# Performance work log

Hardware: AMD Instinct MI355X
Metric: run time of the kernel (lower is better)

Reference implementation:

```python
import jax, jax.numpy as jnp
import numpy as np

NUM_NODES = 100000
NUM_NEIGHS = 64
FEAT = 128
BATCH = 16384
NUM_SAMPLES = 16


def setup_inputs() -> dict:
    key = jax.random.key(0)
    k_ids, k_feat, k_adj = jax.random.split(key, 3)
    ids = jax.random.randint(k_ids, (BATCH,), 0, NUM_NODES, dtype=jnp.int64 if jax.config.jax_enable_x64 else jnp.int32)
    features = jax.random.normal(k_feat, (NUM_NODES, FEAT), dtype=jnp.float32)
    adj_info = jax.random.randint(k_adj, (NUM_NODES, NUM_NEIGHS), 0, NUM_NODES, dtype=jnp.int32)
    return {
        "ids": ids,
        "num_samples": NUM_SAMPLES,
        "features": features,
        "batch_size": BATCH,
        "adj_info": adj_info,
    }


def reference(ids, num_samples, features, batch_size, adj_info):
    # Gather adjacency rows and center-node features
    adj_lists = jnp.take(adj_info, ids, axis=0)            # [B, K]
    node_features = jnp.take(features, ids, axis=0)        # [B, F]
    neighbor_feature = jnp.take(features, adj_lists, axis=0)  # [B, K, F]
    # Euclidean distance center -> each neighbor (broadcast instead of tile)
    diff = node_features[:, None, :] - neighbor_feature    # [B, K, F]
    distance = jnp.sqrt(jnp.sum(diff * diff, axis=-1))     # [B, K]
    prob = jnp.exp(-distance)
    prob = prob / jnp.sum(prob, axis=-1, keepdims=True)    # [B, K]
    # Categorical sampling of num_samples neighbors per row
    logits = jnp.log(prob)
    skey = jax.random.key(42)
    samples_idx = jax.random.categorical(skey, logits, axis=-1, shape=(num_samples, batch_size)).T  # [B, S]
    selected = jnp.take_along_axis(adj_lists, samples_idx, axis=1)  # [B, S]
    return selected
```

## Files before the change

kernel.cpp:

```cpp
#include <hip/hip_runtime.h>
#include <stdint.h>

#define NB 16384
#define NK 64
#define NF 128
#define NS 16
#define RPB 4

__device__ __forceinline__ float xla_exp_f32(float x_in) {
#pragma clang fp contract(off)
  const float exp_hi = 88.3762626647950f;
  const float exp_lo = -88.3762626647949f;
  const float log2ef = 1.44269504088896341f;
  const float c1 = 0.693359375f;
  const float c2 = -2.12194440e-4f;
  const float p0 = 1.9875691500E-4f;
  const float p1 = 1.3981999507E-3f;
  const float p2 = 8.3334519073E-3f;
  const float p3 = 4.1665795894E-2f;
  const float p4 = 1.6666665459E-1f;
  const float p5 = 5.0000001201E-1f;

  float x = fminf(fmaxf(x_in, exp_lo), exp_hi);
  float fx = floorf(fmaf(x, log2ef, 0.5f));
  float tmp = c1 * fx;
  float z2 = c2 * fx;
  x = x - tmp;
  x = x - z2;
  float z = x * x;
  float y = fmaf(x, p0, p1);
  y = fmaf(y, x, p2);
  y = fmaf(y, x, p3);
  y = fmaf(y, x, p4);
  y = fmaf(y, x, p5);
  y = fmaf(y, z, x);
  y = y + 1.0f;
  int n = (int)fx;
  float two_n = __int_as_float((n + 127) << 23);
  return fmaxf(y * two_n, x_in);
}

__device__ __forceinline__ float xla_log_f32(float x_in) {
#pragma clang fp contract(off)
  const float sqrthf = 0.707106781186547524f;
  const float p0 = 7.0376836292E-2f;
  const float p1 = -1.1514610310E-1f;
  const float p2 = 1.1676998740E-1f;
  const float p3 = -1.2420140846E-1f;
  const float p4 = 1.4249322787E-1f;
  const float p5 = -1.6668057665E-1f;
  const float p6 = 2.0000714765E-1f;
  const float p7 = -2.4999993993E-1f;
  const float p8 = 3.3333331174E-1f;
  const float q1 = -2.12194440e-4f;
  const float q2 = 0.693359375f;

  float t = fmaxf(x_in, __uint_as_float(0x00800000u));
  uint32_t bits = __float_as_uint(t);
  float e = (float)((int)(bits >> 23) - 0x7f) + 1.0f;
  float m = __uint_as_float((bits & 0x007fffffu) | 0x3f000000u);
  bool lt = (m < sqrthf);
  float madd = lt ? m : 0.0f;
  e = e - (lt ? 1.0f : 0.0f);
  m = (m + madd) - 1.0f;

  float z = m * m;
  float y = fmaf(m, p0, p1);
  y = fmaf(y, m, p2);
  y = fmaf(y, m, p3);
  y = fmaf(y, m, p4);
  y = fmaf(y, m, p5);
  y = fmaf(y, m, p6);
  y = fmaf(y, m, p7);
  y = fmaf(y, m, p8);
  y = y * m;
  y = y * z;
  y = fmaf(e, q1, y);
  y = y - 0.5f * z;
  float r = m + y;
  r = fmaf(e, q2, r);
  return r;
}

__device__ __forceinline__ void threefry2x32_k42(uint32_t c0, uint32_t c1,
                                                 uint32_t& o0, uint32_t& o1) {
  const uint32_t k0 = 0u, k1 = 42u;
  const uint32_t k2 = k0 ^ k1 ^ 0x1BD11BDAu;
  uint32_t x0 = c0 + k0, x1 = c1 + k1;
#define TF_R(r) { x0 += x1; x1 = (x1 << (r)) | (x1 >> (32 - (r))); x1 ^= x0; }
  TF_R(13) TF_R(15) TF_R(26) TF_R(6)
  x0 += k1; x1 += k2 + 1u;
  TF_R(17) TF_R(29) TF_R(16) TF_R(24)
  x0 += k2; x1 += k0 + 2u;
  TF_R(13) TF_R(15) TF_R(26) TF_R(6)
  x0 += k0; x1 += k1 + 3u;
  TF_R(17) TF_R(29) TF_R(16) TF_R(24)
  x0 += k1; x1 += k2 + 4u;
  TF_R(13) TF_R(15) TF_R(26) TF_R(6)
  x0 += k2; x1 += k0 + 5u;
#undef TF_R
  o0 = x0; o1 = x1;
}

__device__ __forceinline__ uint32_t jax_random_bits32(uint32_t m) {
  uint32_t a, b;
  threefry2x32_k42(0u, m, a, b);
  return a ^ b;
}

__device__ __forceinline__ float gumbel_from_bits(uint32_t bits) {
#pragma clang fp contract(off)
  const float tiny = 1.17549435e-38f;
  float f = __uint_as_float((bits >> 9) | 0x3f800000u) - 1.0f;
  float u = fmaxf(tiny, f + tiny);
  return -xla_log_f32(-xla_log_f32(u));
}

__global__ void __launch_bounds__(256)
dns_kernel(const int* __restrict__ ids, const float* __restrict__ features,
           const int* __restrict__ adj, int* __restrict__ out) {
#pragma clang fp contract(off)
  __shared__ __align__(16) char sbuf[RPB][8192];
  __shared__ __align__(16) float fc[RPB][NF];
  __shared__ __align__(16) float esh[RPB][NK];
  __shared__ int nsh[RPB][NK];
  __shared__ float zb[RPB][NS][4];
  __shared__ int ib[RPB][NS][4];

  const int wave = threadIdx.x >> 6;
  const int k = threadIdx.x & 63;
  const int b = blockIdx.x * RPB + wave;
  const int center = ids[b];

  if (k < NF / 4)
    ((float4*)fc[wave])[k] = ((const float4*)(features + (size_t)center * NF))[k];
  nsh[wave][k] = adj[(size_t)center * NK + k];
  asm volatile("s_waitcnt lgkmcnt(0)" ::: "memory");

  const int rg = k >> 3;
  const int eg = k & 7;
  float acc = 0.0f;
#pragma unroll 1
  for (int q = 0; q < 4; ++q) {
#pragma unroll
    for (int i = 0; i < 8; ++i) {
      const int r = i * 8 + rg;
      const int rn = nsh[wave][r];
      const int esrc = eg ^ (r & 7);
      const float4* g = (const float4*)features + ((size_t)rn * (NF / 4) + q * 8 + esrc);
      __builtin_amdgcn_global_load_lds(
          (const __attribute__((address_space(1))) void*)g,
          (__attribute__((address_space(3))) void*)(sbuf[wave] + i * 1024),
          16, 0, 0);
    }
    asm volatile("s_waitcnt vmcnt(0)" ::: "memory");
#pragma unroll
    for (int j2 = 0; j2 < 8; ++j2) {
      const float4 v = *(const float4*)(sbuf[wave] + k * 128 + ((j2 ^ (k & 7)) << 4));
      const int j = q * 8 + j2;
      float d0 = fc[wave][4 * j + 0] - v.x; acc = acc + d0 * d0;
      float d1 = fc[wave][4 * j + 1] - v.y; acc = acc + d1 * d1;
      float d2 = fc[wave][4 * j + 2] - v.z; acc = acc + d2 * d2;
      float d3 = fc[wave][4 * j + 3] - v.w; acc = acc + d3 * d3;
    }
    asm volatile("s_waitcnt lgkmcnt(0)" ::: "memory");
  }

  const float ev = xla_exp_f32(-sqrtf(acc));
  esh[wave][k] = ev;
  asm volatile("s_waitcnt lgkmcnt(0)" ::: "memory");

  float s = 0.0f;
  const float4* e4 = (const float4*)esh[wave];
#pragma unroll
  for (int i = 0; i < NK / 4; ++i) {
    float4 v = e4[i];
    s = s + v.x; s = s + v.y; s = s + v.z; s = s + v.w;
  }
  const float logit = xla_log_f32(ev / s);

  float (*zsh)[NK + 1] = (float (*)[NK + 1])(void*)sbuf[wave];
#pragma unroll
  for (int ss = 0; ss < NS; ++ss) {
    uint32_t m = (uint32_t)((ss * NB + b) * NK + k);
    zsh[ss][k] = gumbel_from_bits(jax_random_bits32(m)) + logit;
  }
  asm volatile("s_waitcnt lgkmcnt(0)" ::: "memory");

  const int samp = k >> 2;
  const int sub = k & 3;
  const int kbase = sub * 16;
  float best = zsh[samp][kbase];
  int bi = kbase;
#pragma unroll 1
  for (int j = 1; j < 16; ++j) {
    const float v = zsh[samp][kbase + j];
    if (v > best) { best = v; bi = kbase + j; }
  }
  zb[wave][samp][sub] = best;
  ib[wave][samp][sub] = bi;
  asm volatile("s_waitcnt lgkmcnt(0)" ::: "memory");

  if (sub == 0) {
    float bb = zb[wave][samp][0];
    int bbi = ib[wave][samp][0];
#pragma unroll
    for (int qq = 1; qq < 4; ++qq) {
      const float v = zb[wave][samp][qq];
      if (v > bb) { bb = v; bbi = ib[wave][samp][qq]; }
    }
    out[b * NS + samp] = nsh[wave][bbi];
  }
}

extern "C" void kernel_launch(void* const* d_in, const int* in_sizes, int n_in,
                              void* d_out, int out_size, void* d_ws, size_t ws_size,
                              hipStream_t stream) {
  const int* ids = (const int*)d_in[0];
  const float* features = (const float*)d_in[2];
  const int* adj = (const int*)d_in[4];
  int* out = (int*)d_out;
  (void)in_sizes; (void)n_in; (void)out_size; (void)d_ws; (void)ws_size;

  dns_kernel<<<dim3(NB / RPB), dim3(64 * RPB), 0, stream>>>(ids, features, adj, out);
}
```

Baseline: 91.85 us.

## Double-buffer neighbor feature gathers into LDS across eight chunks

Measured after the change: 103.8 us. 1.13x slower.

```diff
diff --git a/kernel.cpp b/kernel.cpp
--- a/kernel.cpp
+++ b/kernel.cpp
@@ -116,6 +116,9 @@
   return -xla_log_f32(-xla_log_f32(u));
 }
 
+#define AS1 __attribute__((address_space(1)))
+#define AS3 __attribute__((address_space(3)))
+
 __global__ void __launch_bounds__(256)
 dns_kernel(const int* __restrict__ ids, const float* __restrict__ features,
            const int* __restrict__ adj, int* __restrict__ out) {
@@ -131,40 +134,61 @@
   const int k = threadIdx.x & 63;
   const int b = blockIdx.x * RPB + wave;
   const int center = ids[b];
+  char* sb = sbuf[wave];
 
   if (k < NF / 4)
     ((float4*)fc[wave])[k] = ((const float4*)(features + (size_t)center * NF))[k];
   nsh[wave][k] = adj[(size_t)center * NK + k];
   asm volatile("s_waitcnt lgkmcnt(0)" ::: "memory");
 
-  const int rg = k >> 3;
-  const int eg = k & 7;
+  const int kq = k >> 2;
+  const int esrc = (k & 3) ^ ((k >> 3) & 3);
+  const float4* f4 = (const float4*)features;
+  const float4* g0 = f4 + (size_t)nsh[wave][0 * 16 + kq] * (NF / 4) + esrc;
+  const float4* g1 = f4 + (size_t)nsh[wave][1 * 16 + kq] * (NF / 4) + esrc;
+  const float4* g2 = f4 + (size_t)nsh[wave][2 * 16 + kq] * (NF / 4) + esrc;
+  const float4* g3 = f4 + (size_t)nsh[wave][3 * 16 + kq] * (NF / 4) + esrc;
+
+#define STAGE(half)                                                         \
+  do {                                                                      \
+    __builtin_amdgcn_global_load_lds((const AS1 void*)g0,                   \
+        (AS3 void*)(sb + (half)), 16, 0, 0);                                \
+    __builtin_amdgcn_global_load_lds((const AS1 void*)g1,                   \
+        (AS3 void*)(sb + (half) + 1024), 16, 0, 0);                         \
+    __builtin_amdgcn_global_load_lds((const AS1 void*)g2,                   \
+        (AS3 void*)(sb + (half) + 2048), 16, 0, 0);                         \
+    __builtin_amdgcn_global_load_lds((const AS1 void*)g3,                   \
+        (AS3 void*)(sb + (half) + 3072), 16, 0, 0);                         \
+    g0 += 4; g1 += 4; g2 += 4; g3 += 4;                                     \
+  } while (0)
+
+  const int S4 = ((k >> 1) & 3) << 4;
+  const float4* fc4 = (const float4*)fc[wave];
   float acc = 0.0f;
+#define CONSUME(cc, half)                                                   \
+  do {                                                                      \
+    const char* rb = sb + (half) + k * 64;                                  \
+    _Pragma("unroll")                                                       \
+    for (int t = 0; t < 4; ++t) {                                           \
+      const float4 v = *(const float4*)(rb + ((t << 4) ^ S4));              \
+      const float4 f = fc4[(cc) * 4 + t];                                   \
+      float d0 = f.x - v.x; acc = acc + d0 * d0;                            \
+      float d1 = f.y - v.y; acc = acc + d1 * d1;                            \
+      float d2 = f.z - v.z; acc = acc + d2 * d2;                            \
+      float d3 = f.w - v.w; acc = acc + d3 * d3;                            \
+    }                                                                       \
+  } while (0)
+
+  STAGE(0);
 #pragma unroll 1
-  for (int q = 0; q < 4; ++q) {
-#pragma unroll
-    for (int i = 0; i < 8; ++i) {
-      const int r = i * 8 + rg;
-      const int rn = nsh[wave][r];
-      const int esrc = eg ^ (r & 7);
-      const float4* g = (const float4*)features + ((size_t)rn * (NF / 4) + q * 8 + esrc);
-      __builtin_amdgcn_global_load_lds(
-          (const __attribute__((address_space(1))) void*)g,
-          (__attribute__((address_space(3))) void*)(sbuf[wave] + i * 1024),
-          16, 0, 0);
-    }
-    asm volatile("s_waitcnt vmcnt(0)" ::: "memory");
-#pragma unroll
-    for (int j2 = 0; j2 < 8; ++j2) {
-      const float4 v = *(const float4*)(sbuf[wave] + k * 128 + ((j2 ^ (k & 7)) << 4));
-      const int j = q * 8 + j2;
-      float d0 = fc[wave][4 * j + 0] - v.x; acc = acc + d0 * d0;
-      float d1 = fc[wave][4 * j + 1] - v.y; acc = acc + d1 * d1;
-      float d2 = fc[wave][4 * j + 2] - v.z; acc = acc + d2 * d2;
-      float d3 = fc[wave][4 * j + 3] - v.w; acc = acc + d3 * d3;
-    }
+  for (int c = 0; c < 7; ++c) {
+    STAGE(((c + 1) & 1) << 12);
+    asm volatile("s_waitcnt vmcnt(4)" ::: "memory");
+    CONSUME(c, (c & 1) << 12);
     asm volatile("s_waitcnt lgkmcnt(0)" ::: "memory");
   }
+  asm volatile("s_waitcnt vmcnt(0)" ::: "memory");
+  CONSUME(7, 4096);
 
   const float ev = xla_exp_f32(-sqrtf(acc));
   esh[wave][k] = ev;
@@ -179,7 +203,7 @@
   }
   const float logit = xla_log_f32(ev / s);
 
-  float (*zsh)[NK + 1] = (float (*)[NK + 1])(void*)sbuf[wave];
+  float (*zsh)[NK + 1] = (float (*)[NK + 1])(void*)sb;
 #pragma unroll
   for (int ss = 0; ss < NS; ++ss) {
     uint32_t m = (uint32_t)((ss * NB + b) * NK + k);
@@ -211,6 +235,8 @@
     }
     out[b * NS + samp] = nsh[wave][bbi];
   }
+#undef STAGE
+#undef CONSUME
 }
 
 extern "C" void kernel_launch(void* const* d_in, const int* in_sizes, int n_in,
```
